# Performance work log

Measured on AMD Instinct MI355X. Metric: run time of the kernel, lower is better.

The kernel has to match this reference:

```python
import jax, jax.numpy as jnp
import numpy as np

B, T = 32768, 32
OBJ_V, PRED_V = 179, 46
E_OBJ, E_PRED, H = 5, 5, 32
IN_DIM = E_OBJ + E_PRED + 2 + 4  # 16, matches LSTMCell input size


def setup_inputs() -> dict:
    key = jax.random.key(0)
    ks = jax.random.split(key, 12)
    s = 0.1
    return {
        "input_objects": jax.random.randint(ks[0], (B, T), 0, OBJ_V),
        "input_boxes": jax.random.uniform(ks[1], (B, T, 4), dtype=jnp.float32),
        "predicates": jax.random.randint(ks[2], (B, T), 0, PRED_V),
        "subject_indicators": jax.random.randint(ks[3], (B, T), 0, 2),
        "target_object": jax.random.randint(ks[4], (B,), 0, OBJ_V),
        "obj_emb": jax.random.normal(ks[5], (OBJ_V, E_OBJ), dtype=jnp.float32) * s,
        "pred_emb": jax.random.normal(ks[6], (PRED_V, E_PRED), dtype=jnp.float32) * s,
        "W_ih": jax.random.normal(ks[7], (4 * H, IN_DIM), dtype=jnp.float32) * s,
        "W_hh": jax.random.normal(ks[8], (4 * H, H), dtype=jnp.float32) * s,
        "b_ih": jnp.zeros((4 * H,), dtype=jnp.float32),
        "b_hh": jnp.zeros((4 * H,), dtype=jnp.float32),
        "fc2_W": jax.random.normal(ks[9], (4, H), dtype=jnp.float32) * s,
        "fc2_b": jnp.zeros((4,), dtype=jnp.float32),
    }


def _forward(input_objects, input_boxes, predicates, subject_indicators,
             obj_emb, pred_emb, W_ih, W_hh, b_ih, b_hh, fc2_W, fc2_b):
    # concatenate_features, vectorized over all timesteps at once: [B,T,16]
    feats = jnp.concatenate([
        obj_emb[input_objects],                                   # [B,T,5]
        pred_emb[predicates],                                     # [B,T,5]
        jax.nn.one_hot(subject_indicators, 2, dtype=jnp.float32), # [B,T,2]
        input_boxes,                                              # [B,T,4]
    ], axis=-1)
    xs = jnp.transpose(feats, (1, 0, 2))  # [T,B,16] for scan over time

    def step(carry, x):
        h, c = carry
        gates = x @ W_ih.T + b_ih + h @ W_hh.T + b_hh  # [B,4H]
        i, f, g, o = jnp.split(gates, 4, axis=-1)      # torch gate order i,f,g,o
        i = jax.nn.sigmoid(i)
        f = jax.nn.sigmoid(f)
        g = jnp.tanh(g)
        o = jax.nn.sigmoid(o)
        c = f * c + i * g
        h = o * jnp.tanh(c)
        return (h, c), None

    h0 = jnp.zeros((input_objects.shape[0], H), dtype=jnp.float32)
    (h, _), _ = jax.lax.scan(step, (h0, h0), xs)
    out = h @ fc2_W.T + fc2_b          # output_fc2 on last hidden state
    return jnp.clip(out, 0.0, 1.0)     # torch.clamp(min=0, max=1)


def reference(input_objects, input_boxes, predicates, subject_indicators, target_object,
              obj_emb, pred_emb, W_ih, W_hh, b_ih, b_hh, fc2_W, fc2_b):
    # target_object is accepted by the torch forward but unused in its body
    return _forward(input_objects, input_boxes, predicates, subject_indicators,
                    obj_emb, pred_emb, W_ih, W_hh, b_ih, b_hh, fc2_W, fc2_b)
```

## Files before the change

kernel.cpp:

```cpp
#include <hip/hip_runtime.h>

#define LDS_BYTES 18720

typedef _Float16 f16x8 __attribute__((ext_vector_type(8)));
typedef float    f32x4 __attribute__((ext_vector_type(4)));

#define LOG2E     1.44269504088896f
#define TWO_LOG2E 2.88539008177793f

__device__ __forceinline__ float sig_pre(float a) {
    return __builtin_amdgcn_rcpf(1.0f + __builtin_amdgcn_exp2f(a));
}
__device__ __forceinline__ float tanh_pre(float a) {
    return 1.0f - 2.0f * __builtin_amdgcn_rcpf(1.0f + __builtin_amdgcn_exp2f(a));
}
__device__ __forceinline__ int pack2(float a, float b) {
    union { _Float16 h[2]; int i; } u;
    u.h[0] = (_Float16)a; u.h[1] = (_Float16)b;
    return u.i;
}

__global__ __launch_bounds__(128, 4)
void lstm_fused(const int* __restrict__ objs,
                const float* __restrict__ boxes,
                const int* __restrict__ preds,
                const int* __restrict__ subj,
                const float* __restrict__ obj_emb,
                const float* __restrict__ pred_emb,
                const float* __restrict__ W_ih,
                const float* __restrict__ W_hh,
                const float* __restrict__ b_ih,
                const float* __restrict__ b_hh,
                const float* __restrict__ fc2_W,
                const float* __restrict__ fc2_b,
                float* __restrict__ out)
{
    extern __shared__ char smem[];
    const int tid  = threadIdx.x;
    const int lane = tid & 63;
    const int wv   = tid >> 6;
    const int quad = lane >> 4;
    const int cidx = lane & 15;
    const int XOFF = 0, HX0 = 16640, HX1 = 17664, ZOFF = 18688;

    if (tid < 8) ((int*)(smem + ZOFF))[tid] = 0;

    {
        int b  = tid >> 3;
        int t0 = (tid & 7) << 2;
        long gb = (long)blockIdx.x * 16 + b;
        int4 ov = *(const int4*)(objs  + gb * 32 + t0);
        int4 pv = *(const int4*)(preds + gb * 32 + t0);
        int4 sv = *(const int4*)(subj  + gb * 32 + t0);
        int oarr[4] = {ov.x, ov.y, ov.z, ov.w};
        int parr[4] = {pv.x, pv.y, pv.z, pv.w};
        int sarr[4] = {sv.x, sv.y, sv.z, sv.w};
        #pragma unroll
        for (int tt = 0; tt < 4; ++tt) {
            int t = t0 + tt;
            const float* eo = obj_emb  + oarr[tt] * 5;
            const float* ep = pred_emb + parr[tt] * 5;
            float4 bx = *(const float4*)(boxes + (gb * 32 + t) * 4);
            f16x8 lo, hi;
            lo[0]=(_Float16)eo[0]; lo[1]=(_Float16)eo[1]; lo[2]=(_Float16)eo[2];
            lo[3]=(_Float16)eo[3]; lo[4]=(_Float16)eo[4];
            lo[5]=(_Float16)ep[0]; lo[6]=(_Float16)ep[1]; lo[7]=(_Float16)ep[2];
            hi[0]=(_Float16)ep[3]; hi[1]=(_Float16)ep[4];
            hi[2]=(_Float16)(sarr[tt]==0 ? 1.0f : 0.0f);
            hi[3]=(_Float16)(sarr[tt]==1 ? 1.0f : 0.0f);
            hi[4]=(_Float16)bx.x; hi[5]=(_Float16)bx.y;
            hi[6]=(_Float16)bx.z; hi[7]=(_Float16)bx.w;
            char* dst = smem + XOFF + b * 1040 + t * 32;
            *(f16x8*)dst        = lo;
            *(f16x8*)(dst + 16) = hi;
        }
    }

    f16x8 Wf[4][2];
    f32x4 bias4[4];
    #pragma unroll
    for (int g = 0; g < 4; ++g) {
        float scale = (g == 2) ? TWO_LOG2E : -LOG2E;
        int um = 8 * (cidx >> 2) + (cidx & 3) + 4 * wv;
        int n  = g * 32 + um;
        #pragma unroll
        for (int ks = 0; ks < 2; ++ks) {
            f16x8 v;
            #pragma unroll
            for (int jj = 0; jj < 8; ++jj) {
                int k = ks * 32 + quad * 8 + jj;
                float val = (k < 16) ? W_ih[n * 16 + k]
                          : (k >= 32) ? W_hh[n * 32 + (k - 32)]
                          : 0.0f;
                v[jj] = (_Float16)(val * scale);
            }
            Wf[g][ks] = v;
        }
        #pragma unroll
        for (int r = 0; r < 4; ++r) {
            int ur = 8 * quad + 4 * wv + r;
            bias4[g][r] = (b_ih[g * 32 + ur] + b_hh[g * 32 + ur]) * scale;
        }
    }

    const bool qlow = (quad < 2);
    int       xaddr = qlow ? (XOFF + cidx * 1040 + quad * 16) : ZOFF;
    const int xinc  = qlow ? 32 : 0;
    const int wr_off = wv * 512 + lane * 8;
    const int rd_off = (1 - wv) * 512 + lane * 8;

    __syncthreads();

    f16x8 xfrag = *(const f16x8*)(smem + xaddr); xaddr += xinc;
    f32x4 accp[4];
    #pragma unroll
    for (int g = 0; g < 4; ++g)
        accp[g] = __builtin_amdgcn_mfma_f32_16x16x32_f16(Wf[g][0], xfrag, bias4[g], 0, 0, 0);

    int pk0 = 0, pk1 = 0;
    int rd0 = 0, rd1 = 0;
    float cst[4] = {0,0,0,0};
    float hr[4];

    #pragma unroll 2
    for (int t = 0; t < 32; ++t) {
        union { int i[4]; f16x8 v; } hf;
        hf.i[0] = wv ? rd0 : pk0;
        hf.i[1] = wv ? rd1 : pk1;
        hf.i[2] = wv ? pk0 : rd0;
        hf.i[3] = wv ? pk1 : rd1;

        f32x4 acc[4];
        #pragma unroll
        for (int g = 0; g < 4; ++g)
            acc[g] = __builtin_amdgcn_mfma_f32_16x16x32_f16(Wf[g][1], hf.v, accp[g], 0, 0, 0);

        f16x8 xn = *(const f16x8*)(smem + xaddr); xaddr += xinc;

        #pragma unroll
        for (int r = 0; r < 4; ++r) {
            float iv = sig_pre(acc[0][r]);
            float fv = sig_pre(acc[1][r]);
            float gv = tanh_pre(acc[2][r]);
            float ov = sig_pre(acc[3][r]);
            float c  = fmaf(fv, cst[r], iv * gv);
            cst[r] = c;
            hr[r] = ov * tanh_pre(c * TWO_LOG2E);
        }
        pk0 = pack2(hr[0], hr[1]);
        pk1 = pack2(hr[2], hr[3]);

        char* buf = smem + ((t & 1) ? HX1 : HX0);
        *(int2*)(buf + wr_off) = (int2){pk0, pk1};

        #pragma unroll
        for (int g = 0; g < 4; ++g)
            accp[g] = __builtin_amdgcn_mfma_f32_16x16x32_f16(Wf[g][0], xn, bias4[g], 0, 0, 0);

        __syncthreads();
        int2 rd = *(const int2*)(buf + rd_off);
        rd0 = rd.x; rd1 = rd.y;
    }

    __syncthreads();
    #pragma unroll
    for (int r = 0; r < 4; ++r)
        *(float*)(smem + cidx * 144 + (8 * quad + 4 * wv + r) * 4) = hr[r];
    __syncthreads();

    if (tid < 64) {
        int b = tid >> 2, jj = tid & 3;
        const float* fw   = fc2_W + jj * 32;
        const float* hrow = (const float*)(smem + b * 144);
        float s = fc2_b[jj];
        #pragma unroll
        for (int k = 0; k < 8; ++k) {
            float4 hv = *(const float4*)(hrow + k * 4);
            s += fw[k*4+0] * hv.x + fw[k*4+1] * hv.y
               + fw[k*4+2] * hv.z + fw[k*4+3] * hv.w;
        }
        s = fminf(fmaxf(s, 0.0f), 1.0f);
        out[(long)blockIdx.x * 64 + tid] = s;
    }
}

extern "C" void kernel_launch(void* const* d_in, const int* in_sizes, int n_in,
                              void* d_out, int out_size, void* d_ws, size_t ws_size,
                              hipStream_t stream)
{
    lstm_fused<<<2048, 128, LDS_BYTES, stream>>>(
        (const int*)d_in[0], (const float*)d_in[1], (const int*)d_in[2],
        (const int*)d_in[3],
        (const float*)d_in[5], (const float*)d_in[6],
        (const float*)d_in[7], (const float*)d_in[8],
        (const float*)d_in[9], (const float*)d_in[10],
        (const float*)d_in[11], (const float*)d_in[12],
        (float*)d_out);
}
```

Baseline: 143.6 us.

## Split LSTM gate tiles across four waves per block instead of two

```diff
diff --git a/kernel.cpp b/kernel.cpp
--- a/kernel.cpp
+++ b/kernel.cpp
@@ -20,7 +20,7 @@
     return u.i;
 }
 
-__global__ __launch_bounds__(128, 4)
+__global__ __launch_bounds__(256, 8)
 void lstm_fused(const int* __restrict__ objs,
                 const float* __restrict__ boxes,
                 const int* __restrict__ preds,
@@ -46,17 +46,17 @@
     if (tid < 8) ((int*)(smem + ZOFF))[tid] = 0;
 
     {
-        int b  = tid >> 3;
-        int t0 = (tid & 7) << 2;
+        int b  = tid >> 4;
+        int t0 = (tid & 15) << 1;
         long gb = (long)blockIdx.x * 16 + b;
-        int4 ov = *(const int4*)(objs  + gb * 32 + t0);
-        int4 pv = *(const int4*)(preds + gb * 32 + t0);
-        int4 sv = *(const int4*)(subj  + gb * 32 + t0);
-        int oarr[4] = {ov.x, ov.y, ov.z, ov.w};
-        int parr[4] = {pv.x, pv.y, pv.z, pv.w};
-        int sarr[4] = {sv.x, sv.y, sv.z, sv.w};
+        int2 ov = *(const int2*)(objs  + gb * 32 + t0);
+        int2 pv = *(const int2*)(preds + gb * 32 + t0);
+        int2 sv = *(const int2*)(subj  + gb * 32 + t0);
+        int oarr[2] = {ov.x, ov.y};
+        int parr[2] = {pv.x, pv.y};
+        int sarr[2] = {sv.x, sv.y};
         #pragma unroll
-        for (int tt = 0; tt < 4; ++tt) {
+        for (int tt = 0; tt < 2; ++tt) {
             int t = t0 + tt;
             const float* eo = obj_emb  + oarr[tt] * 5;
             const float* ep = pred_emb + parr[tt] * 5;
@@ -76,13 +76,15 @@
         }
     }
 
-    f16x8 Wf[4][2];
-    f32x4 bias4[4];
+    f16x8 Wf[2][2];
+    f32x4 bias4[2];
     #pragma unroll
-    for (int g = 0; g < 4; ++g) {
-        float scale = (g == 2) ? TWO_LOG2E : -LOG2E;
-        int um = 8 * (cidx >> 2) + (cidx & 3) + 4 * wv;
-        int n  = g * 32 + um;
+    for (int tile = 0; tile < 2; ++tile) {
+        int rm   = cidx & 3;
+        int u    = 8 * (cidx >> 2) + 2 * wv + (rm & 1);
+        int gate = tile * 2 + (rm >> 1);
+        float scale = (gate == 2) ? TWO_LOG2E : -LOG2E;
+        int n = gate * 32 + u;
         #pragma unroll
         for (int ks = 0; ks < 2; ++ks) {
             f16x8 v;
@@ -94,78 +96,75 @@
                           : 0.0f;
                 v[jj] = (_Float16)(val * scale);
             }
-            Wf[g][ks] = v;
+            Wf[tile][ks] = v;
         }
         #pragma unroll
         for (int r = 0; r < 4; ++r) {
-            int ur = 8 * quad + 4 * wv + r;
-            bias4[g][r] = (b_ih[g * 32 + ur] + b_hh[g * 32 + ur]) * scale;
+            int ur = 8 * quad + 2 * wv + (r & 1);
+            int gr = tile * 2 + (r >> 1);
+            float sc = (gr == 2) ? TWO_LOG2E : -LOG2E;
+            bias4[tile][r] = (b_ih[gr * 32 + ur] + b_hh[gr * 32 + ur]) * sc;
         }
     }
 
     const bool qlow = (quad < 2);
     int       xaddr = qlow ? (XOFF + cidx * 1040 + quad * 16) : ZOFF;
     const int xinc  = qlow ? 32 : 0;
-    const int wr_off = wv * 512 + lane * 8;
-    const int rd_off = (1 - wv) * 512 + lane * 8;
+    const int slot  = lane * 4;
 
     __syncthreads();
 
     f16x8 xfrag = *(const f16x8*)(smem + xaddr); xaddr += xinc;
-    f32x4 accp[4];
+    f32x4 accp[2];
     #pragma unroll
-    for (int g = 0; g < 4; ++g)
-        accp[g] = __builtin_amdgcn_mfma_f32_16x16x32_f16(Wf[g][0], xfrag, bias4[g], 0, 0, 0);
+    for (int tile = 0; tile < 2; ++tile)
+        accp[tile] = __builtin_amdgcn_mfma_f32_16x16x32_f16(Wf[tile][0], xfrag, bias4[tile], 0, 0, 0);
 
-    int pk0 = 0, pk1 = 0;
-    int rd0 = 0, rd1 = 0;
-    float cst[4] = {0,0,0,0};
-    float hr[4];
+    union { int i[4]; f16x8 v; } hf;
+    hf.i[0] = 0; hf.i[1] = 0; hf.i[2] = 0; hf.i[3] = 0;
+    float cst[2] = {0, 0};
+    float h0, h1;
 
     #pragma unroll 2
     for (int t = 0; t < 32; ++t) {
-        union { int i[4]; f16x8 v; } hf;
-        hf.i[0] = wv ? rd0 : pk0;
-        hf.i[1] = wv ? rd1 : pk1;
-        hf.i[2] = wv ? pk0 : rd0;
-        hf.i[3] = wv ? pk1 : rd1;
-
-        f32x4 acc[4];
-        #pragma unroll
-        for (int g = 0; g < 4; ++g)
-            acc[g] = __builtin_amdgcn_mfma_f32_16x16x32_f16(Wf[g][1], hf.v, accp[g], 0, 0, 0);
+        f32x4 acc0 = __builtin_amdgcn_mfma_f32_16x16x32_f16(Wf[0][1], hf.v, accp[0], 0, 0, 0);
+        f32x4 acc1 = __builtin_amdgcn_mfma_f32_16x16x32_f16(Wf[1][1], hf.v, accp[1], 0, 0, 0);
 
         f16x8 xn = *(const f16x8*)(smem + xaddr); xaddr += xinc;
 
-        #pragma unroll
-        for (int r = 0; r < 4; ++r) {
-            float iv = sig_pre(acc[0][r]);
-            float fv = sig_pre(acc[1][r]);
-            float gv = tanh_pre(acc[2][r]);
-            float ov = sig_pre(acc[3][r]);
-            float c  = fmaf(fv, cst[r], iv * gv);
-            cst[r] = c;
-            hr[r] = ov * tanh_pre(c * TWO_LOG2E);
-        }
-        pk0 = pack2(hr[0], hr[1]);
-        pk1 = pack2(hr[2], hr[3]);
+        float i0 = sig_pre(acc0[0]);
+        float i1 = sig_pre(acc0[1]);
+        float f0 = sig_pre(acc0[2]);
+        float f1 = sig_pre(acc0[3]);
+        float g0 = tanh_pre(acc1[0]);
+        float g1 = tanh_pre(acc1[1]);
+        float o0 = sig_pre(acc1[2]);
+        float o1 = sig_pre(acc1[3]);
+        float c0 = fmaf(f0, cst[0], i0 * g0);
+        float c1 = fmaf(f1, cst[1], i1 * g1);
+        cst[0] = c0; cst[1] = c1;
+        h0 = o0 * tanh_pre(c0 * TWO_LOG2E);
+        h1 = o1 * tanh_pre(c1 * TWO_LOG2E);
+        int pk = pack2(h0, h1);
 
         char* buf = smem + ((t & 1) ? HX1 : HX0);
-        *(int2*)(buf + wr_off) = (int2){pk0, pk1};
+        *(int*)(buf + wv * 256 + slot) = pk;
 
-        #pragma unroll
-        for (int g = 0; g < 4; ++g)
-            accp[g] = __builtin_amdgcn_mfma_f32_16x16x32_f16(Wf[g][0], xn, bias4[g], 0, 0, 0);
+        accp[0] = __builtin_amdgcn_mfma_f32_16x16x32_f16(Wf[0][0], xn, bias4[0], 0, 0, 0);
+        accp[1] = __builtin_amdgcn_mfma_f32_16x16x32_f16(Wf[1][0], xn, bias4[1], 0, 0, 0);
 
         __syncthreads();
-        int2 rd = *(const int2*)(buf + rd_off);
-        rd0 = rd.x; rd1 = rd.y;
+        hf.i[0] = *(const int*)(buf + 0   + slot);
+        hf.i[1] = *(const int*)(buf + 256 + slot);
+        hf.i[2] = *(const int*)(buf + 512 + slot);
+        hf.i[3] = *(const int*)(buf + 768 + slot);
     }
 
     __syncthreads();
-    #pragma unroll
-    for (int r = 0; r < 4; ++r)
-        *(float*)(smem + cidx * 144 + (8 * quad + 4 * wv + r) * 4) = hr[r];
+    {
+        int u0 = 8 * quad + 2 * wv;
+        *(float2*)(smem + cidx * 144 + u0 * 4) = (float2){h0, h1};
+    }
     __syncthreads();
 
     if (tid < 64) {
@@ -188,7 +187,7 @@
                               void* d_out, int out_size, void* d_ws, size_t ws_size,
                               hipStream_t stream)
 {
-    lstm_fused<<<2048, 128, LDS_BYTES, stream>>>(
+    lstm_fused<<<2048, 256, LDS_BYTES, stream>>>(
         (const int*)d_in[0], (const float*)d_in[1], (const int*)d_in[2],
         (const int*)d_in[3],
         (const float*)d_in[5], (const float*)d_in[6],
```

Result: faster. 138.3 us (-3.7%).
